# Kernel tuning notes

Hardware: AMD Instinct MI355X
Metric: run time of the kernel (lower is better)

Reference implementation:

```python
import jax, jax.numpy as jnp
import numpy as np

DIM = 512

def setup_inputs() -> dict:
    key = jax.random.key(0)
    ks = jax.random.split(key, 7)
    B, Nq, Nkv = 8, 1024, 4096
    prototype = jax.random.normal(ks[0], (B, Nq, DIM), dtype=jnp.float32)
    q_x = jax.random.normal(ks[1], (B, Nkv, DIM), dtype=jnp.float32)
    qry_attn_mask = jax.random.bernoulli(ks[2], 0.5, (B, Nkv))  # True = keep
    # Linear(dim, dim, bias=False) weights, torch convention y = x @ W.T
    s = 1.0 / np.sqrt(DIM)
    Wq = jax.random.uniform(ks[3], (DIM, DIM), jnp.float32, -s, s)
    Wk = jax.random.uniform(ks[4], (DIM, DIM), jnp.float32, -s, s)
    Wv = jax.random.uniform(ks[5], (DIM, DIM), jnp.float32, -s, s)
    Wproj = jax.random.uniform(ks[6], (DIM, DIM), jnp.float32, -s, s)
    return {"prototype": prototype, "q_x": q_x, "qry_attn_mask": qry_attn_mask,
            "Wq": Wq, "Wk": Wk, "Wv": Wv, "Wproj": Wproj}

def reference(prototype, q_x, qry_attn_mask, Wq, Wk, Wv, Wproj):
    scale = DIM ** (-0.5)
    q = jnp.einsum('bnd,ed->bne', prototype, Wq)          # [B,Nq,D]
    k = jnp.einsum('bmd,ed->bme', q_x, Wk)                # [B,Nkv,D]
    v = jnp.einsum('bmd,ed->bme', q_x, Wv)                # [B,Nkv,D]
    attn = jnp.einsum('bnd,bmd->bnm', q, k) * scale       # [B,Nq,Nkv]
    bias = (~qry_attn_mask).astype(attn.dtype)[:, None, :] * -10000.0
    attn = jax.nn.softmax(attn + bias, axis=-1)
    x = jnp.einsum('bnm,bmd->bnd', attn, v)
    x = jnp.einsum('bnd,ed->bne', x, Wproj)
    return x
```

## Files before the change

### kernel.cpp

```cpp
#include <hip/hip_runtime.h>
#include <hip/hip_bf16.h>
#include <stdint.h>


typedef __bf16 bf16;
typedef bf16 bf16x8 __attribute__((ext_vector_type(8)));
typedef bf16 bf16x4 __attribute__((ext_vector_type(4)));
typedef float f32x4 __attribute__((ext_vector_type(4)));

#define NB 8
#define NQ 1024
#define NKV 4096
#define DD 512
#define RT_LD 136

__device__ __forceinline__ void lds16(const bf16* g, bf16* l) {
  __builtin_amdgcn_global_load_lds(
      (const __attribute__((address_space(1))) unsigned int*)g,
      (__attribute__((address_space(3))) unsigned int*)l, 16, 0, 0);
}

__global__ void scan_mask(const void* __restrict__ mask,
                          int* __restrict__ idx, int* __restrict__ cnt,
                          int* __restrict__ kpad, float* __restrict__ denom) {
  const int b = blockIdx.x, tid = threadIdx.x;
  for (int i = tid; i < NQ; i += 256) denom[b * NQ + i] = 0.f;

  __shared__ int s0, s1;
  if (tid == 0) { s0 = 0; s1 = 0; }
  __syncthreads();
  {
    const unsigned* mw = (const unsigned*)mask;
    int b0 = 0, b1 = 0;
    for (int i = tid; i < 8192; i += 256) {
      unsigned v = mw[i];
      if (v > 1u) b0 = 1;
      if (v != 0u && v != 0x3F800000u) b1 = 1;
    }
    if (b0) atomicOr(&s0, 1);
    if (b1) atomicOr(&s1, 1);
  }
  __syncthreads();
  const int mode = (s0 == 0) ? 0 : ((s1 == 0) ? 1 : 2);

  __shared__ int ps[256];
  unsigned bits = 0;
  int c = 0;
  const int base = tid * 16;
  for (int i = 0; i < 16; ++i) {
    const int col = base + i;
    bool k;
    if (mode == 0)      k = ((const int*)mask)[b * NKV + col] != 0;
    else if (mode == 1) k = ((const float*)mask)[b * NKV + col] != 0.f;
    else                k = ((const unsigned char*)mask)[b * NKV + col] != 0;
    bits |= (unsigned)k << i;
    c += k;
  }
  ps[tid] = c;
  __syncthreads();
  for (int s = 1; s < 256; s <<= 1) {
    int v = (tid >= s) ? ps[tid - s] : 0;
    __syncthreads();
    ps[tid] += v;
    __syncthreads();
  }
  int off = ps[tid] - c;
  for (int i = 0; i < 16; ++i)
    if ((bits >> i) & 1) idx[b * NKV + off++] = base + i;
  if (tid == 255) {
    cnt[b] = ps[255];
    kpad[b] = (ps[255] + 127) & ~127;
  }
}

__global__ void prep(const float* __restrict__ qx, const int* __restrict__ idx,
                     const int* __restrict__ cnt, const int* __restrict__ kpad,
                     bf16* __restrict__ qc,
                     const float* __restrict__ proto, bf16* __restrict__ proto_b,
                     const float* __restrict__ Wq, const float* __restrict__ Wk,
                     const float* __restrict__ Wv, const float* __restrict__ Wp,
                     bf16* __restrict__ Wq_b, bf16* __restrict__ Wkv_b,
                     bf16* __restrict__ Wp_b) {
  const int blk = blockIdx.x, tid = threadIdx.x;
  if (blk < 2048) {
    const int b = blk >> 8, bx = blk & 255;
    const int wave = tid >> 6, lane = tid & 63;
    const int r0 = bx * 16 + wave * 4;
    const int n = cnt[b];
    const int kp = kpad[b];
#pragma unroll
    for (int j = 0; j < 4; ++j) {
      const int row = r0 + j;
      if (row >= kp) return;
      bf16x4* d = (bf16x4*)(qc + ((long)b * NKV + row) * DD) + lane;
      if (row < n) {
        const int src = idx[b * NKV + row];
        const float4* s = (const float4*)(qx + ((long)b * NKV + src) * DD) + lane;
        float4 v0 = s[0], v1 = s[64];
        bf16x4 o0, o1;
        o0.x = (bf16)v0.x; o0.y = (bf16)v0.y; o0.z = (bf16)v0.z; o0.w = (bf16)v0.w;
        o1.x = (bf16)v1.x; o1.y = (bf16)v1.y; o1.z = (bf16)v1.z; o1.w = (bf16)v1.w;
        d[0] = o0;
        d[64] = o1;
      } else {
        bf16x4 z;
        z.x = (bf16)0.f; z.y = (bf16)0.f; z.z = (bf16)0.f; z.w = (bf16)0.f;
        d[0] = z;
        d[64] = z;
      }
    }
  } else if (blk < 6144) {
    const int i = (blk - 2048) * 256 + tid;
    float4 v = ((const float4*)proto)[i];
    bf16x4 o;
    o.x = (bf16)v.x; o.y = (bf16)v.y; o.z = (bf16)v.z; o.w = (bf16)v.w;
    ((bf16x4*)proto_b)[i] = o;
  } else {
    const int j = (blk - 6144) * 256 + tid;
    const int w = j >> 16, r = j & 65535;
    const float* src = (w == 0) ? Wq : (w == 1) ? Wk : (w == 2) ? Wv : Wp;
    bf16x4* dst = (w == 0) ? (bf16x4*)Wq_b
                : (w == 3) ? (bf16x4*)Wp_b
                           : (bf16x4*)Wkv_b + (w == 2 ? 65536 : 0);
    float4 v = ((const float4*)src)[r];
    bf16x4 o;
    o.x = (bf16)v.x; o.y = (bf16)v.y; o.z = (bf16)v.z; o.w = (bf16)v.w;
    dst[r] = o;
  }
}

template <int EPI>
__global__ void __launch_bounds__(256, 2)
gemm_bt(const bf16* __restrict__ A, const bf16* __restrict__ Bw,
        void* __restrict__ Cp, void* __restrict__ Cp2,
        int N, int Klen, int Kstride,
        long sA, long sB, long sC,
        const int* __restrict__ cnt, const int* __restrict__ kpad,
        float* __restrict__ denom, float scale, int M) {
  __shared__ alignas(16) bf16 Smem[128 * RT_LD];
  bf16* As = Smem;
  bf16* Bs = Smem + 8192;
  bf16* Rt = Smem;
  const int tid = threadIdx.x;
  const int wave = tid >> 6, lane = tid & 63;
  const int l15 = lane & 15, l4 = lane >> 4;
  const int wm = (wave >> 1) * 64, wn = (wave & 1) * 64;
  const int bx = (EPI == 5) ? blockIdx.y : blockIdx.x;
  const int by = (EPI == 5) ? blockIdx.x : blockIdx.y;
  const int b = blockIdx.z;

  if constexpr (EPI == 2) {
    if (bx * 128 >= kpad[b]) return;
  } else if constexpr (EPI == 5) {
    const int bb = by >> 5, loc = (by & 31) * 128;
    if (loc >= kpad[bb]) return;
  }

  const bf16* Ab = A + (long)b * sA + (long)(by * 128) * Kstride;
  const bf16* Bb = Bw + (long)b * sB + (long)(bx * 128) * Kstride;

  const int srow = lane >> 2, scol = (lane & 3) * 8;
  const bf16* ag[4];
  const bf16* bg[4];
  bf16* al[4];
  bf16* bl[4];
#pragma unroll
  for (int i = 0; i < 4; ++i) {
    const int st = wave * 4 + i, rs = st >> 1, cs = st & 1;
    ag[i] = Ab + (long)(rs * 16 + srow) * Kstride + cs * 32 + scol;
    bg[i] = Bb + (long)(rs * 16 + srow) * Kstride + cs * 32 + scol;
    al[i] = As + st * 512;
    bl[i] = Bs + st * 512;
  }

  f32x4 acc[4][4] = {};

  for (int kt = 0; kt < Klen; kt += 64) {
    __syncthreads();
#pragma unroll
    for (int i = 0; i < 4; ++i) lds16(ag[i], al[i]);
#pragma unroll
    for (int i = 0; i < 4; ++i) lds16(bg[i], bl[i]);
#pragma unroll
    for (int i = 0; i < 4; ++i) { ag[i] += 64; bg[i] += 64; }
    __syncthreads();
    bf16x8 af0[4], af1[4], bf0[4], bf1[4];
    const int ra = (wave >> 1) * 4, rb = (wave & 1) * 4;
#pragma unroll
    for (int t = 0; t < 4; ++t) {
      af0[t] = *(const bf16x8*)(As + ((ra + t) * 2 + 0) * 512 + l15 * 32 + l4 * 8);
      af1[t] = *(const bf16x8*)(As + ((ra + t) * 2 + 1) * 512 + l15 * 32 + l4 * 8);
      bf0[t] = *(const bf16x8*)(Bs + ((rb + t) * 2 + 0) * 512 + l15 * 32 + l4 * 8);
      bf1[t] = *(const bf16x8*)(Bs + ((rb + t) * 2 + 1) * 512 + l15 * 32 + l4 * 8);
    }
#pragma unroll
    for (int mt = 0; mt < 4; ++mt)
#pragma unroll
      for (int nt = 0; nt < 4; ++nt) {
        acc[mt][nt] = __builtin_amdgcn_mfma_f32_16x16x32_bf16(af0[mt], bf0[nt],
                                                              acc[mt][nt], 0, 0, 0);
        acc[mt][nt] = __builtin_amdgcn_mfma_f32_16x16x32_bf16(af1[mt], bf1[nt],
                                                              acc[mt][nt], 0, 0, 0);
      }
  }

  const int rowBase = by * 128 + wm;
  const int colBase = bx * 128 + wn;
  const int tR = by * 128;
  const int tC = bx * 128;

  __syncthreads();

  if constexpr (EPI == 2) {
    bf16* C = (bf16*)Cp + (long)b * sC;
    const int nkeep = cnt[b];
    float rs[4][4];
#pragma unroll
    for (int mt = 0; mt < 4; ++mt)
#pragma unroll
      for (int r = 0; r < 4; ++r) rs[mt][r] = 0.f;
#pragma unroll
    for (int nt = 0; nt < 4; ++nt) {
      const bool keep = (colBase + nt * 16 + l15) < nkeep;
#pragma unroll
      for (int mt = 0; mt < 4; ++mt)
#pragma unroll
        for (int r = 0; r < 4; ++r) {
          float p = keep ? __expf(acc[mt][nt][r] * scale) : 0.f;
          rs[mt][r] += p;
          Rt[(wm + mt * 16 + l4 * 4 + r) * RT_LD + wn + nt * 16 + l15] = (bf16)p;
        }
    }
#pragma unroll
    for (int mt = 0; mt < 4; ++mt)
#pragma unroll
      for (int r = 0; r < 4; ++r) {
        float v = rs[mt][r];
        v += __shfl_xor(v, 1, 64);
        v += __shfl_xor(v, 2, 64);
        v += __shfl_xor(v, 4, 64);
        v += __shfl_xor(v, 8, 64);
        if (l15 == 0)
          atomicAdd(&denom[b * M + rowBase + mt * 16 + l4 * 4 + r], v);
      }
    __syncthreads();
    const int r0 = tid >> 2, cq = (tid & 3) * 32;
#pragma unroll
    for (int h = 0; h < 128; h += 64)
#pragma unroll
      for (int j = 0; j < 4; ++j) {
        bf16x8 v = *(const bf16x8*)(Rt + (r0 + h) * RT_LD + cq + j * 8);
        *(bf16x8*)(C + (long)(tR + r0 + h) * N + tC + cq + j * 8) = v;
      }
  } else if constexpr (EPI == 0) {
    bf16* C = (bf16*)Cp;
#pragma unroll
    for (int mt = 0; mt < 4; ++mt)
#pragma unroll
      for (int nt = 0; nt < 4; ++nt)
#pragma unroll
        for (int r = 0; r < 4; ++r)
          Rt[(wm + mt * 16 + l4 * 4 + r) * RT_LD + wn + nt * 16 + l15] =
              (bf16)acc[mt][nt][r];
    __syncthreads();
    const int r0 = tid >> 2, cq = (tid & 3) * 32;
#pragma unroll
    for (int h = 0; h < 128; h += 64)
#pragma unroll
      for (int j = 0; j < 4; ++j) {
        bf16x8 v = *(const bf16x8*)(Rt + (r0 + h) * RT_LD + cq + j * 8);
        *(bf16x8*)(C + (long)(tR + r0 + h) * N + tC + cq + j * 8) = v;
      }
  } else if constexpr (EPI == 4) {
    float* C = (float*)Cp;
#pragma unroll
    for (int mt = 0; mt < 4; ++mt)
#pragma unroll
      for (int nt = 0; nt < 4; ++nt)
#pragma unroll
        for (int r = 0; r < 4; ++r)
          C[(long)(tR + wm + mt * 16 + l4 * 4 + r) * N + tC + wn + nt * 16 + l15] =
              acc[mt][nt][r];
  } else {
    if (tC < 512) {
      bf16* C = (bf16*)Cp;
#pragma unroll
      for (int mt = 0; mt < 4; ++mt)
#pragma unroll
        for (int nt = 0; nt < 4; ++nt)
#pragma unroll
          for (int r = 0; r < 4; ++r)
            Rt[(wm + mt * 16 + l4 * 4 + r) * RT_LD + wn + nt * 16 + l15] =
                (bf16)acc[mt][nt][r];
      __syncthreads();
      const int r0 = tid >> 2, cq = (tid & 3) * 32;
#pragma unroll
      for (int h = 0; h < 128; h += 64)
#pragma unroll
        for (int j = 0; j < 4; ++j) {
          bf16x8 v = *(const bf16x8*)(Rt + (r0 + h) * RT_LD + cq + j * 8);
          *(bf16x8*)(C + (long)(tR + r0 + h) * 512 + tC + cq + j * 8) = v;
        }
    } else {
      bf16* C = (bf16*)Cp2;
#pragma unroll
      for (int mt = 0; mt < 4; ++mt) {
        const int r0 = wm + mt * 16 + l4 * 4;
#pragma unroll
        for (int nt = 0; nt < 4; ++nt) {
          const int cloc = wn + nt * 16 + l15;
          bf16x4 o;
          o.x = (bf16)acc[mt][nt][0]; o.y = (bf16)acc[mt][nt][1];
          o.z = (bf16)acc[mt][nt][2]; o.w = (bf16)acc[mt][nt][3];
          *(bf16x4*)(Rt + cloc * RT_LD + r0) = o;
        }
      }
      __syncthreads();
      const int bb = tR >> 12, kvloc = tR & 4095;
      const int d0 = tid >> 2, kvq = (tid & 3) * 32;
#pragma unroll
      for (int h = 0; h < 128; h += 64)
#pragma unroll
        for (int j = 0; j < 4; ++j) {
          bf16x8 v = *(const bf16x8*)(Rt + (d0 + h) * RT_LD + kvq + j * 8);
          *(bf16x8*)(C + (long)bb * DD * NKV + (long)(tC - 512 + d0 + h) * NKV +
                     kvloc + kvq + j * 8) = v;
        }
    }
  }
}

__global__ void __launch_bounds__(256, 4)
pv_direct(const bf16* __restrict__ P, const bf16* __restrict__ vT,
          const float* __restrict__ denom, const int* __restrict__ kpad,
          bf16* __restrict__ x) {
  __shared__ alignas(16) bf16 Smem[12288];
  bf16* As = Smem;
  bf16* Bs = Smem + 4096;
  bf16* Rt = Smem;
  const int tid = threadIdx.x;
  const int wave = tid >> 6, lane = tid & 63;
  const int l15 = lane & 15, l4 = lane >> 4;
  const int wm = (wave >> 1) * 32, wn = (wave & 1) * 64;
  const int qB = blockIdx.x * 64;
  const int dB = blockIdx.y * 128;
  const int b = blockIdx.z;
  const int Kb = kpad[b];

  const bf16* Ab = P + (long)b * NQ * NKV + (long)qB * NKV;
  const bf16* Bb = vT + (long)b * DD * NKV + (long)dB * NKV;

  const int srow = lane >> 2, scol = (lane & 3) * 8;
  const bf16* ag[2];
  const bf16* bg[4];
  bf16* al[2];
  bf16* bl[4];
#pragma unroll
  for (int i = 0; i < 2; ++i) {
    const int st = wave * 2 + i, rs = st >> 1, cs = st & 1;
    ag[i] = Ab + (long)(rs * 16 + srow) * NKV + cs * 32 + scol;
    al[i] = As + st * 512;
  }
#pragma unroll
  for (int i = 0; i < 4; ++i) {
    const int st = wave * 4 + i, rs = st >> 1, cs = st & 1;
    bg[i] = Bb + (long)(rs * 16 + srow) * NKV + cs * 32 + scol;
    bl[i] = Bs + st * 512;
  }

  f32x4 acc[2][4] = {};

  for (int kt = 0; kt < Kb; kt += 64) {
    __syncthreads();
#pragma unroll
    for (int i = 0; i < 2; ++i) lds16(ag[i], al[i]);
#pragma unroll
    for (int i = 0; i < 4; ++i) lds16(bg[i], bl[i]);
#pragma unroll
    for (int i = 0; i < 2; ++i) ag[i] += 64;
#pragma unroll
    for (int i = 0; i < 4; ++i) bg[i] += 64;
    __syncthreads();
    bf16x8 af0[2], af1[2], bf0[4], bf1[4];
    const int ra = (wave >> 1) * 2, rb = (wave & 1) * 4;
#pragma unroll
    for (int t = 0; t < 2; ++t) {
      af0[t] = *(const bf16x8*)(As + ((ra + t) * 2 + 0) * 512 + l15 * 32 + l4 * 8);
      af1[t] = *(const bf16x8*)(As + ((ra + t) * 2 + 1) * 512 + l15 * 32 + l4 * 8);
    }
#pragma unroll
    for (int t = 0; t < 4; ++t) {
      bf0[t] = *(const bf16x8*)(Bs + ((rb + t) * 2 + 0) * 512 + l15 * 32 + l4 * 8);
      bf1[t] = *(const bf16x8*)(Bs + ((rb + t) * 2 + 1) * 512 + l15 * 32 + l4 * 8);
    }
#pragma unroll
    for (int mt = 0; mt < 2; ++mt)
#pragma unroll
      for (int nt = 0; nt < 4; ++nt) {
        acc[mt][nt] = __builtin_amdgcn_mfma_f32_16x16x32_bf16(af0[mt], bf0[nt],
                                                              acc[mt][nt], 0, 0, 0);
        acc[mt][nt] = __builtin_amdgcn_mfma_f32_16x16x32_bf16(af1[mt], bf1[nt],
                                                              acc[mt][nt], 0, 0, 0);
      }
  }

  __syncthreads();
#pragma unroll
  for (int mt = 0; mt < 2; ++mt)
#pragma unroll
    for (int r = 0; r < 4; ++r) {
      const int row = wm + mt * 16 + l4 * 4 + r;
      const float inv = 1.0f / denom[b * NQ + qB + row];
#pragma unroll
      for (int nt = 0; nt < 4; ++nt)
        Rt[row * RT_LD + wn + nt * 16 + l15] = (bf16)(acc[mt][nt][r] * inv);
    }
  __syncthreads();
  const int r0 = tid >> 2, cq = (tid & 3) * 32;
#pragma unroll
  for (int j = 0; j < 4; ++j) {
    bf16x8 v = *(const bf16x8*)(Rt + r0 * RT_LD + cq + j * 8);
    *(bf16x8*)(x + (long)(b * NQ + qB + r0) * DD + dB + cq + j * 8) = v;
  }
}

extern "C" void kernel_launch(void* const* d_in, const int* in_sizes, int n_in,
                              void* d_out, int out_size, void* d_ws, size_t ws_size,
                              hipStream_t stream) {
  const float* proto = (const float*)d_in[0];
  const float* qx    = (const float*)d_in[1];
  const void*  mask  = d_in[2];
  const float* Wq    = (const float*)d_in[3];
  const float* Wk    = (const float*)d_in[4];
  const float* Wv    = (const float*)d_in[5];
  const float* Wproj = (const float*)d_in[6];
  float* out = (float*)d_out;

  char* w = (char*)d_ws;
  int*   cnt   = (int*)(w + 64);
  int*   kpadA = (int*)(w + 128);
  float* denom = (float*)(w + 4096);
  size_t off = 65536;
  bf16* Wq_b  = (bf16*)(w + off); off += (size_t)DD * DD * 2;
  bf16* Wkv_b = (bf16*)(w + off); off += (size_t)DD * DD * 4;
  bf16* Wp_b  = (bf16*)(w + off); off += (size_t)DD * DD * 2;
  int*  idx   = (int*)(w + off);  off += (size_t)NB * NKV * 4;
  bf16* q_b   = (bf16*)(w + off); off += (size_t)NB * NQ * DD * 2;
  bf16* k_b   = (bf16*)(w + off); off += (size_t)NB * NKV * DD * 2;
  bf16* vT_b  = (bf16*)(w + off); off += (size_t)NB * NKV * DD * 2;
  bf16* x_b   = (bf16*)(w + off); off += (size_t)NB * NQ * DD * 2;
  size_t off_pp = off;
  bf16* proto_b = (bf16*)(w + off); off += (size_t)NB * NQ * DD * 2;
  bf16* qc_b    = (bf16*)(w + off);
  bf16* P       = (bf16*)(w + off_pp);

  scan_mask<<<8, 256, 0, stream>>>(mask, idx, cnt, kpadA, denom);
  prep<<<7168, 256, 0, stream>>>(qx, idx, cnt, kpadA, qc_b,
                                 proto, proto_b, Wq, Wk, Wv, Wproj,
                                 Wq_b, Wkv_b, Wp_b);

  const float scale = 0.04419417382415922f;

  gemm_bt<0><<<dim3(4, 64, 1), 256, 0, stream>>>(
      proto_b, Wq_b, q_b, nullptr, DD, DD, DD, 0L, 0L, 0L,
      cnt, kpadA, nullptr, 0.f, 0);
  gemm_bt<5><<<dim3(256, 8, 1), 256, 0, stream>>>(
      qc_b, Wkv_b, k_b, vT_b, 1024, DD, DD, 0L, 0L, 0L,
      cnt, kpadA, nullptr, 0.f, 0);
  gemm_bt<2><<<dim3(NKV / 128, NQ / 128, NB), 256, 0, stream>>>(
      q_b, k_b, P, nullptr, NKV, DD, DD,
      (long)NQ * DD, (long)NKV * DD, (long)NQ * NKV,
      cnt, kpadA, denom, scale, NQ);
  pv_direct<<<dim3(16, 4, 8), 256, 0, stream>>>(P, vT_b, denom, kpadA, x_b);
  gemm_bt<4><<<dim3(4, 64, 1), 256, 0, stream>>>(
      x_b, Wp_b, out, nullptr, DD, DD, DD, 0L, 0L, 0L,
      cnt, kpadA, nullptr, 0.f, 0);
}
```

Baseline: 313.8 us.

## Double-buffer LDS tiles in gemm_bt and pv_direct to overlap loads with MFMA

Both GEMM kernels now prefetch the next K tile into a second LDS buffer while the current tile is being consumed by MFMAs. This uses one barrier per iteration instead of two. The aim is to hide global-to-LDS load latency behind compute. In exchange, shared memory per block doubles and pv_direct's launch-bounds occupancy hint drops from 4 to 3, which may reduce how many blocks are resident.

```diff
diff --git a/kernel.cpp b/kernel.cpp
--- a/kernel.cpp
+++ b/kernel.cpp
@@ -129,6 +129,7 @@
   }
 }
 
+#define GB_DBUF 16384
 template <int EPI>
 __global__ void __launch_bounds__(256, 2)
 gemm_bt(const bf16* __restrict__ A, const bf16* __restrict__ Bw,
@@ -137,7 +138,7 @@
         long sA, long sB, long sC,
         const int* __restrict__ cnt, const int* __restrict__ kpad,
         float* __restrict__ denom, float scale, int M) {
-  __shared__ alignas(16) bf16 Smem[128 * RT_LD];
+  __shared__ alignas(16) bf16 Smem[32768];
   bf16* As = Smem;
   bf16* Bs = Smem + 8192;
   bf16* Rt = Smem;
@@ -175,23 +176,35 @@
 
   f32x4 acc[4][4] = {};
 
+#pragma unroll
+  for (int i = 0; i < 4; ++i) lds16(ag[i], al[i]);
+#pragma unroll
+  for (int i = 0; i < 4; ++i) lds16(bg[i], bl[i]);
+#pragma unroll
+  for (int i = 0; i < 4; ++i) { ag[i] += 64; bg[i] += 64; }
+  __syncthreads();
+
+  int cur = 0;
   for (int kt = 0; kt < Klen; kt += 64) {
-    __syncthreads();
-#pragma unroll
-    for (int i = 0; i < 4; ++i) lds16(ag[i], al[i]);
-#pragma unroll
-    for (int i = 0; i < 4; ++i) lds16(bg[i], bl[i]);
-#pragma unroll
-    for (int i = 0; i < 4; ++i) { ag[i] += 64; bg[i] += 64; }
-    __syncthreads();
+    const bf16* Ac = As + cur * GB_DBUF;
+    const bf16* Bc = Bs + cur * GB_DBUF;
     bf16x8 af0[4], af1[4], bf0[4], bf1[4];
     const int ra = (wave >> 1) * 4, rb = (wave & 1) * 4;
 #pragma unroll
     for (int t = 0; t < 4; ++t) {
-      af0[t] = *(const bf16x8*)(As + ((ra + t) * 2 + 0) * 512 + l15 * 32 + l4 * 8);
-      af1[t] = *(const bf16x8*)(As + ((ra + t) * 2 + 1) * 512 + l15 * 32 + l4 * 8);
-      bf0[t] = *(const bf16x8*)(Bs + ((rb + t) * 2 + 0) * 512 + l15 * 32 + l4 * 8);
-      bf1[t] = *(const bf16x8*)(Bs + ((rb + t) * 2 + 1) * 512 + l15 * 32 + l4 * 8);
+      af0[t] = *(const bf16x8*)(Ac + ((ra + t) * 2 + 0) * 512 + l15 * 32 + l4 * 8);
+      af1[t] = *(const bf16x8*)(Ac + ((ra + t) * 2 + 1) * 512 + l15 * 32 + l4 * 8);
+      bf0[t] = *(const bf16x8*)(Bc + ((rb + t) * 2 + 0) * 512 + l15 * 32 + l4 * 8);
+      bf1[t] = *(const bf16x8*)(Bc + ((rb + t) * 2 + 1) * 512 + l15 * 32 + l4 * 8);
+    }
+    if (kt + 64 < Klen) {
+      const int nb = (cur ^ 1) * GB_DBUF;
+#pragma unroll
+      for (int i = 0; i < 4; ++i) lds16(ag[i], al[i] + nb);
+#pragma unroll
+      for (int i = 0; i < 4; ++i) lds16(bg[i], bl[i] + nb);
+#pragma unroll
+      for (int i = 0; i < 4; ++i) { ag[i] += 64; bg[i] += 64; }
     }
 #pragma unroll
     for (int mt = 0; mt < 4; ++mt)
@@ -202,14 +215,14 @@
         acc[mt][nt] = __builtin_amdgcn_mfma_f32_16x16x32_bf16(af1[mt], bf1[nt],
                                                               acc[mt][nt], 0, 0, 0);
       }
+    __syncthreads();
+    cur ^= 1;
   }
 
   const int rowBase = by * 128 + wm;
   const int colBase = bx * 128 + wn;
   const int tR = by * 128;
   const int tC = bx * 128;
-
-  __syncthreads();
 
   if constexpr (EPI == 2) {
     bf16* C = (bf16*)Cp + (long)b * sC;
@@ -330,11 +343,12 @@
   }
 }
 
-__global__ void __launch_bounds__(256, 4)
+#define PV_DBUF 12288
+__global__ void __launch_bounds__(256, 3)
 pv_direct(const bf16* __restrict__ P, const bf16* __restrict__ vT,
           const float* __restrict__ denom, const int* __restrict__ kpad,
           bf16* __restrict__ x) {
-  __shared__ alignas(16) bf16 Smem[12288];
+  __shared__ alignas(16) bf16 Smem[24576];
   bf16* As = Smem;
   bf16* Bs = Smem + 4096;
   bf16* Rt = Smem;
@@ -370,28 +384,42 @@
 
   f32x4 acc[2][4] = {};
 
+#pragma unroll
+  for (int i = 0; i < 2; ++i) lds16(ag[i], al[i]);
+#pragma unroll
+  for (int i = 0; i < 4; ++i) lds16(bg[i], bl[i]);
+#pragma unroll
+  for (int i = 0; i < 2; ++i) ag[i] += 64;
+#pragma unroll
+  for (int i = 0; i < 4; ++i) bg[i] += 64;
+  __syncthreads();
+
+  int cur = 0;
   for (int kt = 0; kt < Kb; kt += 64) {
-    __syncthreads();
-#pragma unroll
-    for (int i = 0; i < 2; ++i) lds16(ag[i], al[i]);
-#pragma unroll
-    for (int i = 0; i < 4; ++i) lds16(bg[i], bl[i]);
-#pragma unroll
-    for (int i = 0; i < 2; ++i) ag[i] += 64;
-#pragma unroll
-    for (int i = 0; i < 4; ++i) bg[i] += 64;
-    __syncthreads();
+    const bf16* Ac = As + cur * PV_DBUF;
+    const bf16* Bc = Bs + cur * PV_DBUF;
     bf16x8 af0[2], af1[2], bf0[4], bf1[4];
     const int ra = (wave >> 1) * 2, rb = (wave & 1) * 4;
 #pragma unroll
     for (int t = 0; t < 2; ++t) {
-      af0[t] = *(const bf16x8*)(As + ((ra + t) * 2 + 0) * 512 + l15 * 32 + l4 * 8);
-      af1[t] = *(const bf16x8*)(As + ((ra + t) * 2 + 1) * 512 + l15 * 32 + l4 * 8);
+      af0[t] = *(const bf16x8*)(Ac + ((ra + t) * 2 + 0) * 512 + l15 * 32 + l4 * 8);
+      af1[t] = *(const bf16x8*)(Ac + ((ra + t) * 2 + 1) * 512 + l15 * 32 + l4 * 8);
     }
 #pragma unroll
     for (int t = 0; t < 4; ++t) {
-      bf0[t] = *(const bf16x8*)(Bs + ((rb + t) * 2 + 0) * 512 + l15 * 32 + l4 * 8);
-      bf1[t] = *(const bf16x8*)(Bs + ((rb + t) * 2 + 1) * 512 + l15 * 32 + l4 * 8);
+      bf0[t] = *(const bf16x8*)(Bc + ((rb + t) * 2 + 0) * 512 + l15 * 32 + l4 * 8);
+      bf1[t] = *(const bf16x8*)(Bc + ((rb + t) * 2 + 1) * 512 + l15 * 32 + l4 * 8);
+    }
+    if (kt + 64 < Kb) {
+      const int nb = (cur ^ 1) * PV_DBUF;
+#pragma unroll
+      for (int i = 0; i < 2; ++i) lds16(ag[i], al[i] + nb);
+#pragma unroll
+      for (int i = 0; i < 4; ++i) lds16(bg[i], bl[i] + nb);
+#pragma unroll
+      for (int i = 0; i < 2; ++i) ag[i] += 64;
+#pragma unroll
+      for (int i = 0; i < 4; ++i) bg[i] += 64;
     }
 #pragma unroll
     for (int mt = 0; mt < 2; ++mt)
@@ -402,9 +430,10 @@
         acc[mt][nt] = __builtin_amdgcn_mfma_f32_16x16x32_bf16(af1[mt], bf1[nt],
                                                               acc[mt][nt], 0, 0, 0);
       }
-  }
-
-  __syncthreads();
+    __syncthreads();
+    cur ^= 1;
+  }
+
 #pragma unroll
   for (int mt = 0; mt < 2; ++mt)
 #pragma unroll
```

Result: slower. 327.8 us (+4.5%).

## Triple-buffer K=32 stages in GEMM and PV kernels with async LDS loads

Applied to the files above, without the earlier changes.

Replaces the single-buffered K=64 load/compute loop in gemm_bt and pv_direct with a three-stage ring of K=32 tiles. Direct-to-LDS loads are issued two stages ahead, with explicit vmcnt waits and a single barrier per step. This is meant to overlap global-memory latency with MFMA work instead of serialising them behind two barriers per iteration. It also raises the gemm launch bound to 3 blocks per CU. The cost is more shared memory per block, and only one barrier per step guards against overwriting a buffer that a slower wave may still be reading.

```diff
diff --git a/kernel.cpp b/kernel.cpp
--- a/kernel.cpp
+++ b/kernel.cpp
@@ -130,16 +130,14 @@
 }
 
 template <int EPI>
-__global__ void __launch_bounds__(256, 2)
+__global__ void __launch_bounds__(256, 3)
 gemm_bt(const bf16* __restrict__ A, const bf16* __restrict__ Bw,
         void* __restrict__ Cp, void* __restrict__ Cp2,
         int N, int Klen, int Kstride,
         long sA, long sB, long sC,
         const int* __restrict__ cnt, const int* __restrict__ kpad,
         float* __restrict__ denom, float scale, int M) {
-  __shared__ alignas(16) bf16 Smem[128 * RT_LD];
-  bf16* As = Smem;
-  bf16* Bs = Smem + 8192;
+  __shared__ alignas(16) bf16 Smem[24576];
   bf16* Rt = Smem;
   const int tid = threadIdx.x;
   const int wave = tid >> 6, lane = tid & 63;
@@ -160,57 +158,64 @@
   const bf16* Bb = Bw + (long)b * sB + (long)(bx * 128) * Kstride;
 
   const int srow = lane >> 2, scol = (lane & 3) * 8;
-  const bf16* ag[4];
-  const bf16* bg[4];
-  bf16* al[4];
-  bf16* bl[4];
-#pragma unroll
-  for (int i = 0; i < 4; ++i) {
-    const int st = wave * 4 + i, rs = st >> 1, cs = st & 1;
-    ag[i] = Ab + (long)(rs * 16 + srow) * Kstride + cs * 32 + scol;
-    bg[i] = Bb + (long)(rs * 16 + srow) * Kstride + cs * 32 + scol;
-    al[i] = As + st * 512;
-    bl[i] = Bs + st * 512;
-  }
+  const int c0 = wave * 2, c1 = wave * 2 + 1;
+  const bf16* g0 = Ab + (long)(c0 * 16 + srow) * Kstride + scol;
+  const bf16* g1 = Ab + (long)(c1 * 16 + srow) * Kstride + scol;
+  const bf16* g2 = Bb + (long)(c0 * 16 + srow) * Kstride + scol;
+  const bf16* g3 = Bb + (long)(c1 * 16 + srow) * Kstride + scol;
+  bf16* l0 = Smem + c0 * 512;
+  bf16* l1 = Smem + c1 * 512;
+  bf16* l2 = Smem + 4096 + c0 * 512;
+  bf16* l3 = Smem + 4096 + c1 * 512;
 
   f32x4 acc[4][4] = {};
-
-  for (int kt = 0; kt < Klen; kt += 64) {
-    __syncthreads();
-#pragma unroll
-    for (int i = 0; i < 4; ++i) lds16(ag[i], al[i]);
-#pragma unroll
-    for (int i = 0; i < 4; ++i) lds16(bg[i], bl[i]);
-#pragma unroll
-    for (int i = 0; i < 4; ++i) { ag[i] += 64; bg[i] += 64; }
-    __syncthreads();
-    bf16x8 af0[4], af1[4], bf0[4], bf1[4];
-    const int ra = (wave >> 1) * 4, rb = (wave & 1) * 4;
-#pragma unroll
-    for (int t = 0; t < 4; ++t) {
-      af0[t] = *(const bf16x8*)(As + ((ra + t) * 2 + 0) * 512 + l15 * 32 + l4 * 8);
-      af1[t] = *(const bf16x8*)(As + ((ra + t) * 2 + 1) * 512 + l15 * 32 + l4 * 8);
-      bf0[t] = *(const bf16x8*)(Bs + ((rb + t) * 2 + 0) * 512 + l15 * 32 + l4 * 8);
-      bf1[t] = *(const bf16x8*)(Bs + ((rb + t) * 2 + 1) * 512 + l15 * 32 + l4 * 8);
+  const int nt = Klen >> 5;
+
+#define GSTAGE(bb)                                            \
+  do {                                                        \
+    const int o_ = (bb) * 8192;                               \
+    lds16(g0, l0 + o_); lds16(g1, l1 + o_);                   \
+    lds16(g2, l2 + o_); lds16(g3, l3 + o_);                   \
+    g0 += 32; g1 += 32; g2 += 32; g3 += 32;                   \
+  } while (0)
+
+  GSTAGE(0);
+  GSTAGE(1);
+  int rd = 0, wr = 2;
+  for (int t = 0; t < nt; ++t) {
+    if (t + 1 < nt) {
+      asm volatile("s_waitcnt vmcnt(4)" ::: "memory");
+    } else {
+      asm volatile("s_waitcnt vmcnt(0)" ::: "memory");
+    }
+    __builtin_amdgcn_s_barrier();
+    __builtin_amdgcn_sched_barrier(0);
+    if (t + 2 < nt) GSTAGE(wr);
+    wr = (wr == 2) ? 0 : wr + 1;
+    const bf16* Ac = Smem + rd * 8192;
+    const bf16* Bc = Ac + 4096;
+    rd = (rd == 2) ? 0 : rd + 1;
+    bf16x8 af[4], bfr[4];
+#pragma unroll
+    for (int t2 = 0; t2 < 4; ++t2) {
+      af[t2]  = *(const bf16x8*)(Ac + (wm + t2 * 16 + l15) * 32 + l4 * 8);
+      bfr[t2] = *(const bf16x8*)(Bc + (wn + t2 * 16 + l15) * 32 + l4 * 8);
     }
 #pragma unroll
     for (int mt = 0; mt < 4; ++mt)
 #pragma unroll
-      for (int nt = 0; nt < 4; ++nt) {
-        acc[mt][nt] = __builtin_amdgcn_mfma_f32_16x16x32_bf16(af0[mt], bf0[nt],
-                                                              acc[mt][nt], 0, 0, 0);
-        acc[mt][nt] = __builtin_amdgcn_mfma_f32_16x16x32_bf16(af1[mt], bf1[nt],
-                                                              acc[mt][nt], 0, 0, 0);
-      }
-  }
+      for (int nt2 = 0; nt2 < 4; ++nt2)
+        acc[mt][nt2] = __builtin_amdgcn_mfma_f32_16x16x32_bf16(af[mt], bfr[nt2],
+                                                               acc[mt][nt2], 0, 0, 0);
+  }
+#undef GSTAGE
+  __syncthreads();
 
   const int rowBase = by * 128 + wm;
   const int colBase = bx * 128 + wn;
   const int tR = by * 128;
   const int tC = bx * 128;
 
-  __syncthreads();
-
   if constexpr (EPI == 2) {
     bf16* C = (bf16*)Cp + (long)b * sC;
     const int nkeep = cnt[b];
@@ -220,15 +225,15 @@
 #pragma unroll
       for (int r = 0; r < 4; ++r) rs[mt][r] = 0.f;
 #pragma unroll
-    for (int nt = 0; nt < 4; ++nt) {
-      const bool keep = (colBase + nt * 16 + l15) < nkeep;
+    for (int nt2 = 0; nt2 < 4; ++nt2) {
+      const bool keep = (colBase + nt2 * 16 + l15) < nkeep;
 #pragma unroll
       for (int mt = 0; mt < 4; ++mt)
 #pragma unroll
         for (int r = 0; r < 4; ++r) {
-          float p = keep ? __expf(acc[mt][nt][r] * scale) : 0.f;
+          float p = keep ? __expf(acc[mt][nt2][r] * scale) : 0.f;
           rs[mt][r] += p;
-          Rt[(wm + mt * 16 + l4 * 4 + r) * RT_LD + wn + nt * 16 + l15] = (bf16)p;
+          Rt[(wm + mt * 16 + l4 * 4 + r) * RT_LD + wn + nt2 * 16 + l15] = (bf16)p;
         }
     }
 #pragma unroll
@@ -257,11 +262,11 @@
 #pragma unroll
     for (int mt = 0; mt < 4; ++mt)
 #pragma unroll
-      for (int nt = 0; nt < 4; ++nt)
+      for (int nt2 = 0; nt2 < 4; ++nt2)
 #pragma unroll
         for (int r = 0; r < 4; ++r)
-          Rt[(wm + mt * 16 + l4 * 4 + r) * RT_LD + wn + nt * 16 + l15] =
-              (bf16)acc[mt][nt][r];
+          Rt[(wm + mt * 16 + l4 * 4 + r) * RT_LD + wn + nt2 * 16 + l15] =
+              (bf16)acc[mt][nt2][r];
     __syncthreads();
     const int r0 = tid >> 2, cq = (tid & 3) * 32;
 #pragma unroll
@@ -276,22 +281,22 @@
 #pragma unroll
     for (int mt = 0; mt < 4; ++mt)
 #pragma unroll
-      for (int nt = 0; nt < 4; ++nt)
+      for (int nt2 = 0; nt2 < 4; ++nt2)
 #pragma unroll
         for (int r = 0; r < 4; ++r)
-          C[(long)(tR + wm + mt * 16 + l4 * 4 + r) * N + tC + wn + nt * 16 + l15] =
-              acc[mt][nt][r];
+          C[(long)(tR + wm + mt * 16 + l4 * 4 + r) * N + tC + wn + nt2 * 16 + l15] =
+              acc[mt][nt2][r];
   } else {
     if (tC < 512) {
       bf16* C = (bf16*)Cp;
 #pragma unroll
       for (int mt = 0; mt < 4; ++mt)
 #pragma unroll
-        for (int nt = 0; nt < 4; ++nt)
+        for (int nt2 = 0; nt2 < 4; ++nt2)
 #pragma unroll
           for (int r = 0; r < 4; ++r)
-            Rt[(wm + mt * 16 + l4 * 4 + r) * RT_LD + wn + nt * 16 + l15] =
-                (bf16)acc[mt][nt][r];
+            Rt[(wm + mt * 16 + l4 * 4 + r) * RT_LD + wn + nt2 * 16 + l15] =
+                (bf16)acc[mt][nt2][r];
       __syncthreads();
       const int r0 = tid >> 2, cq = (tid & 3) * 32;
 #pragma unroll
@@ -307,11 +312,11 @@
       for (int mt = 0; mt < 4; ++mt) {
         const int r0 = wm + mt * 16 + l4 * 4;
 #pragma unroll
-        for (int nt = 0; nt < 4; ++nt) {
-          const int cloc = wn + nt * 16 + l15;
+        for (int nt2 = 0; nt2 < 4; ++nt2) {
+          const int cloc = wn + nt2 * 16 + l15;
           bf16x4 o;
-          o.x = (bf16)acc[mt][nt][0]; o.y = (bf16)acc[mt][nt][1];
-          o.z = (bf16)acc[mt][nt][2]; o.w = (bf16)acc[mt][nt][3];
+          o.x = (bf16)acc[mt][nt2][0]; o.y = (bf16)acc[mt][nt2][1];
+          o.z = (bf16)acc[mt][nt2][2]; o.w = (bf16)acc[mt][nt2][3];
           *(bf16x4*)(Rt + cloc * RT_LD + r0) = o;
         }
       }
@@ -334,9 +339,7 @@
 pv_direct(const bf16* __restrict__ P, const bf16* __restrict__ vT,
           const float* __restrict__ denom, const int* __restrict__ kpad,
           bf16* __restrict__ x) {
-  __shared__ alignas(16) bf16 Smem[12288];
-  bf16* As = Smem;
-  bf16* Bs = Smem + 4096;
+  __shared__ alignas(16) bf16 Smem[18432];
   bf16* Rt = Smem;
   const int tid = threadIdx.x;
   const int wave = tid >> 6, lane = tid & 63;
@@ -351,60 +354,58 @@
   const bf16* Bb = vT + (long)b * DD * NKV + (long)dB * NKV;
 
   const int srow = lane >> 2, scol = (lane & 3) * 8;
-  const bf16* ag[2];
-  const bf16* bg[4];
-  bf16* al[2];
-  bf16* bl[4];
-#pragma unroll
-  for (int i = 0; i < 2; ++i) {
-    const int st = wave * 2 + i, rs = st >> 1, cs = st & 1;
-    ag[i] = Ab + (long)(rs * 16 + srow) * NKV + cs * 32 + scol;
-    al[i] = As + st * 512;
-  }
-#pragma unroll
-  for (int i = 0; i < 4; ++i) {
-    const int st = wave * 4 + i, rs = st >> 1, cs = st & 1;
-    bg[i] = Bb + (long)(rs * 16 + srow) * NKV + cs * 32 + scol;
-    bl[i] = Bs + st * 512;
-  }
+  const int c0 = wave * 2, c1 = wave * 2 + 1;
+  const bf16* ga  = Ab + (long)(wave * 16 + srow) * NKV + scol;
+  const bf16* gb0 = Bb + (long)(c0 * 16 + srow) * NKV + scol;
+  const bf16* gb1 = Bb + (long)(c1 * 16 + srow) * NKV + scol;
+  bf16* la  = Smem + wave * 512;
+  bf16* lb0 = Smem + 2048 + c0 * 512;
+  bf16* lb1 = Smem + 2048 + c1 * 512;
 
   f32x4 acc[2][4] = {};
-
-  for (int kt = 0; kt < Kb; kt += 64) {
-    __syncthreads();
-#pragma unroll
-    for (int i = 0; i < 2; ++i) lds16(ag[i], al[i]);
-#pragma unroll
-    for (int i = 0; i < 4; ++i) lds16(bg[i], bl[i]);
-#pragma unroll
-    for (int i = 0; i < 2; ++i) ag[i] += 64;
-#pragma unroll
-    for (int i = 0; i < 4; ++i) bg[i] += 64;
-    __syncthreads();
-    bf16x8 af0[2], af1[2], bf0[4], bf1[4];
-    const int ra = (wave >> 1) * 2, rb = (wave & 1) * 4;
-#pragma unroll
-    for (int t = 0; t < 2; ++t) {
-      af0[t] = *(const bf16x8*)(As + ((ra + t) * 2 + 0) * 512 + l15 * 32 + l4 * 8);
-      af1[t] = *(const bf16x8*)(As + ((ra + t) * 2 + 1) * 512 + l15 * 32 + l4 * 8);
-    }
-#pragma unroll
-    for (int t = 0; t < 4; ++t) {
-      bf0[t] = *(const bf16x8*)(Bs + ((rb + t) * 2 + 0) * 512 + l15 * 32 + l4 * 8);
-      bf1[t] = *(const bf16x8*)(Bs + ((rb + t) * 2 + 1) * 512 + l15 * 32 + l4 * 8);
-    }
+  const int nt = Kb >> 5;
+
+#define PSTAGE(bb)                                           \
+  do {                                                       \
+    const int o_ = (bb) * 6144;                              \
+    lds16(ga, la + o_); lds16(gb0, lb0 + o_);                \
+    lds16(gb1, lb1 + o_);                                    \
+    ga += 32; gb0 += 32; gb1 += 32;                          \
+  } while (0)
+
+  PSTAGE(0);
+  PSTAGE(1);
+  int rd = 0, wr = 2;
+  for (int t = 0; t < nt; ++t) {
+    if (t + 1 < nt) {
+      asm volatile("s_waitcnt vmcnt(3)" ::: "memory");
+    } else {
+      asm volatile("s_waitcnt vmcnt(0)" ::: "memory");
+    }
+    __builtin_amdgcn_s_barrier();
+    __builtin_amdgcn_sched_barrier(0);
+    if (t + 2 < nt) PSTAGE(wr);
+    wr = (wr == 2) ? 0 : wr + 1;
+    const bf16* Ac = Smem + rd * 6144;
+    const bf16* Bc = Ac + 2048;
+    rd = (rd == 2) ? 0 : rd + 1;
+    bf16x8 af[2], bfr[4];
+#pragma unroll
+    for (int t2 = 0; t2 < 2; ++t2)
+      af[t2] = *(const bf16x8*)(Ac + (wm + t2 * 16 + l15) * 32 + l4 * 8);
+#pragma unroll
+    for (int t2 = 0; t2 < 4; ++t2)
+      bfr[t2] = *(const bf16x8*)(Bc + (wn + t2 * 16 + l15) * 32 + l4 * 8);
 #pragma unroll
     for (int mt = 0; mt < 2; ++mt)
 #pragma unroll
-      for (int nt = 0; nt < 4; ++nt) {
-        acc[mt][nt] = __builtin_amdgcn_mfma_f32_16x16x32_bf16(af0[mt], bf0[nt],
-                                                              acc[mt][nt], 0, 0, 0);
-        acc[mt][nt] = __builtin_amdgcn_mfma_f32_16x16x32_bf16(af1[mt], bf1[nt],
-                                                              acc[mt][nt], 0, 0, 0);
-      }
-  }
-
-  __syncthreads();
+      for (int nt2 = 0; nt2 < 4; ++nt2)
+        acc[mt][nt2] = __builtin_amdgcn_mfma_f32_16x16x32_bf16(af[mt], bfr[nt2],
+                                                               acc[mt][nt2], 0, 0, 0);
+  }
+#undef PSTAGE
+  __syncthreads();
+
 #pragma unroll
   for (int mt = 0; mt < 2; ++mt)
 #pragma unroll
@@ -412,8 +413,8 @@
       const int row = wm + mt * 16 + l4 * 4 + r;
       const float inv = 1.0f / denom[b * NQ + qB + row];
 #pragma unroll
-      for (int nt = 0; nt < 4; ++nt)
-        Rt[row * RT_LD + wn + nt * 16 + l15] = (bf16)(acc[mt][nt][r] * inv);
+      for (int nt2 = 0; nt2 < 4; ++nt2)
+        Rt[row * RT_LD + wn + nt2 * 16 + l15] = (bf16)(acc[mt][nt2][r] * inv);
     }
   __syncthreads();
   const int r0 = tid >> 2, cq = (tid & 3) * 32;
```

After: 308.3 us. No clear change (-1.7%).

## Halve K-tile to 32 and split epilogue staging to cut LDS for occupancy

Applied to the files above, without the earlier changes.

Both GEMM kernels now stage a K-depth of 32 instead of 64 per iteration, shrinking the A/B LDS buffers. The epilogues write the 128x128 result tile through LDS in two 64-row (or 64-column) halves so the staging buffer fits in the smaller allocation. Launch bounds are raised to 6 blocks per CU to use the freed LDS for more resident waves. The cost is twice as many barrier-separated loop iterations with less MFMA work per barrier, extra barriers in the epilogue, and tighter per-thread register budgets that may cause spills.

```diff
diff --git a/kernel.cpp b/kernel.cpp
--- a/kernel.cpp
+++ b/kernel.cpp
@@ -130,16 +130,16 @@
 }
 
 template <int EPI>
-__global__ void __launch_bounds__(256, 2)
+__global__ void __launch_bounds__(256, 6)
 gemm_bt(const bf16* __restrict__ A, const bf16* __restrict__ Bw,
         void* __restrict__ Cp, void* __restrict__ Cp2,
         int N, int Klen, int Kstride,
         long sA, long sB, long sC,
         const int* __restrict__ cnt, const int* __restrict__ kpad,
         float* __restrict__ denom, float scale, int M) {
-  __shared__ alignas(16) bf16 Smem[128 * RT_LD];
+  __shared__ alignas(16) bf16 Smem[8704];
   bf16* As = Smem;
-  bf16* Bs = Smem + 8192;
+  bf16* Bs = Smem + 4096;
   bf16* Rt = Smem;
   const int tid = threadIdx.x;
   const int wave = tid >> 6, lane = tid & 63;
@@ -159,55 +159,48 @@
   const bf16* Ab = A + (long)b * sA + (long)(by * 128) * Kstride;
   const bf16* Bb = Bw + (long)b * sB + (long)(bx * 128) * Kstride;
 
-  const int srow = lane >> 2, scol = (lane & 3) * 8;
-  const bf16* ag[4];
-  const bf16* bg[4];
-  bf16* al[4];
-  bf16* bl[4];
-#pragma unroll
-  for (int i = 0; i < 4; ++i) {
-    const int st = wave * 4 + i, rs = st >> 1, cs = st & 1;
-    ag[i] = Ab + (long)(rs * 16 + srow) * Kstride + cs * 32 + scol;
-    bg[i] = Bb + (long)(rs * 16 + srow) * Kstride + cs * 32 + scol;
-    al[i] = As + st * 512;
-    bl[i] = Bs + st * 512;
-  }
+  const int c0 = wave * 2, c1 = wave * 2 + 1;
+  const int srow = lane >> 2;
+  const int scol = (lane & 3) * 8;
+  const bf16* ag0 = Ab + (long)(c0 * 16 + srow) * Kstride + scol;
+  const bf16* ag1 = Ab + (long)(c1 * 16 + srow) * Kstride + scol;
+  const bf16* bg0 = Bb + (long)(c0 * 16 + srow) * Kstride + scol;
+  const bf16* bg1 = Bb + (long)(c1 * 16 + srow) * Kstride + scol;
+  bf16* al0 = As + c0 * 512;
+  bf16* al1 = As + c1 * 512;
+  bf16* bl0 = Bs + c0 * 512;
+  bf16* bl1 = Bs + c1 * 512;
 
   f32x4 acc[4][4] = {};
 
-  for (int kt = 0; kt < Klen; kt += 64) {
-    __syncthreads();
-#pragma unroll
-    for (int i = 0; i < 4; ++i) lds16(ag[i], al[i]);
-#pragma unroll
-    for (int i = 0; i < 4; ++i) lds16(bg[i], bl[i]);
-#pragma unroll
-    for (int i = 0; i < 4; ++i) { ag[i] += 64; bg[i] += 64; }
-    __syncthreads();
-    bf16x8 af0[4], af1[4], bf0[4], bf1[4];
-    const int ra = (wave >> 1) * 4, rb = (wave & 1) * 4;
-#pragma unroll
-    for (int t = 0; t < 4; ++t) {
-      af0[t] = *(const bf16x8*)(As + ((ra + t) * 2 + 0) * 512 + l15 * 32 + l4 * 8);
-      af1[t] = *(const bf16x8*)(As + ((ra + t) * 2 + 1) * 512 + l15 * 32 + l4 * 8);
-      bf0[t] = *(const bf16x8*)(Bs + ((rb + t) * 2 + 0) * 512 + l15 * 32 + l4 * 8);
-      bf1[t] = *(const bf16x8*)(Bs + ((rb + t) * 2 + 1) * 512 + l15 * 32 + l4 * 8);
-    }
+  for (int kt = 0; kt < Klen; kt += 32) {
+    __syncthreads();
+    lds16(ag0, al0);
+    lds16(ag1, al1);
+    lds16(bg0, bl0);
+    lds16(bg1, bl1);
+    ag0 += 32; ag1 += 32; bg0 += 32; bg1 += 32;
+    __syncthreads();
+    bf16x8 af[4], bfr[4];
+#pragma unroll
+    for (int t = 0; t < 4; ++t)
+      af[t] = *(const bf16x8*)(As + (wm + t * 16 + l15) * 32 + l4 * 8);
+#pragma unroll
+    for (int t = 0; t < 4; ++t)
+      bfr[t] = *(const bf16x8*)(Bs + (wn + t * 16 + l15) * 32 + l4 * 8);
 #pragma unroll
     for (int mt = 0; mt < 4; ++mt)
 #pragma unroll
-      for (int nt = 0; nt < 4; ++nt) {
-        acc[mt][nt] = __builtin_amdgcn_mfma_f32_16x16x32_bf16(af0[mt], bf0[nt],
+      for (int nt = 0; nt < 4; ++nt)
+        acc[mt][nt] = __builtin_amdgcn_mfma_f32_16x16x32_bf16(af[mt], bfr[nt],
                                                               acc[mt][nt], 0, 0, 0);
-        acc[mt][nt] = __builtin_amdgcn_mfma_f32_16x16x32_bf16(af1[mt], bf1[nt],
-                                                              acc[mt][nt], 0, 0, 0);
-      }
   }
 
   const int rowBase = by * 128 + wm;
   const int colBase = bx * 128 + wn;
   const int tR = by * 128;
   const int tC = bx * 128;
+  const int r0 = tid >> 2, cq = (tid & 3) * 32;
 
   __syncthreads();
 
@@ -225,11 +218,8 @@
 #pragma unroll
       for (int mt = 0; mt < 4; ++mt)
 #pragma unroll
-        for (int r = 0; r < 4; ++r) {
-          float p = keep ? __expf(acc[mt][nt][r] * scale) : 0.f;
-          rs[mt][r] += p;
-          Rt[(wm + mt * 16 + l4 * 4 + r) * RT_LD + wn + nt * 16 + l15] = (bf16)p;
-        }
+        for (int r = 0; r < 4; ++r)
+          rs[mt][r] += keep ? __expf(acc[mt][nt][r] * scale) : 0.f;
     }
 #pragma unroll
     for (int mt = 0; mt < 4; ++mt)
@@ -243,34 +233,51 @@
         if (l15 == 0)
           atomicAdd(&denom[b * M + rowBase + mt * 16 + l4 * 4 + r], v);
       }
-    __syncthreads();
-    const int r0 = tid >> 2, cq = (tid & 3) * 32;
-#pragma unroll
-    for (int h = 0; h < 128; h += 64)
+#pragma unroll
+    for (int ph = 0; ph < 2; ++ph) {
+      if (wm == ph * 64) {
+#pragma unroll
+        for (int nt = 0; nt < 4; ++nt) {
+          const bool keep = (colBase + nt * 16 + l15) < nkeep;
+#pragma unroll
+          for (int mt = 0; mt < 4; ++mt)
+#pragma unroll
+            for (int r = 0; r < 4; ++r) {
+              float p = keep ? __expf(acc[mt][nt][r] * scale) : 0.f;
+              Rt[(mt * 16 + l4 * 4 + r) * RT_LD + wn + nt * 16 + l15] = (bf16)p;
+            }
+        }
+      }
+      __syncthreads();
 #pragma unroll
       for (int j = 0; j < 4; ++j) {
-        bf16x8 v = *(const bf16x8*)(Rt + (r0 + h) * RT_LD + cq + j * 8);
-        *(bf16x8*)(C + (long)(tR + r0 + h) * N + tC + cq + j * 8) = v;
-      }
+        bf16x8 v = *(const bf16x8*)(Rt + r0 * RT_LD + cq + j * 8);
+        *(bf16x8*)(C + (long)(tR + ph * 64 + r0) * N + tC + cq + j * 8) = v;
+      }
+      __syncthreads();
+    }
   } else if constexpr (EPI == 0) {
     bf16* C = (bf16*)Cp;
 #pragma unroll
-    for (int mt = 0; mt < 4; ++mt)
-#pragma unroll
-      for (int nt = 0; nt < 4; ++nt)
-#pragma unroll
-        for (int r = 0; r < 4; ++r)
-          Rt[(wm + mt * 16 + l4 * 4 + r) * RT_LD + wn + nt * 16 + l15] =
-              (bf16)acc[mt][nt][r];
-    __syncthreads();
-    const int r0 = tid >> 2, cq = (tid & 3) * 32;
-#pragma unroll
-    for (int h = 0; h < 128; h += 64)
+    for (int ph = 0; ph < 2; ++ph) {
+      if (wm == ph * 64) {
+#pragma unroll
+        for (int mt = 0; mt < 4; ++mt)
+#pragma unroll
+          for (int nt = 0; nt < 4; ++nt)
+#pragma unroll
+            for (int r = 0; r < 4; ++r)
+              Rt[(mt * 16 + l4 * 4 + r) * RT_LD + wn + nt * 16 + l15] =
+                  (bf16)acc[mt][nt][r];
+      }
+      __syncthreads();
 #pragma unroll
       for (int j = 0; j < 4; ++j) {
-        bf16x8 v = *(const bf16x8*)(Rt + (r0 + h) * RT_LD + cq + j * 8);
-        *(bf16x8*)(C + (long)(tR + r0 + h) * N + tC + cq + j * 8) = v;
-      }
+        bf16x8 v = *(const bf16x8*)(Rt + r0 * RT_LD + cq + j * 8);
+        *(bf16x8*)(C + (long)(tR + ph * 64 + r0) * N + tC + cq + j * 8) = v;
+      }
+      __syncthreads();
+    }
   } else if constexpr (EPI == 4) {
     float* C = (float*)Cp;
 #pragma unroll
@@ -285,58 +292,64 @@
     if (tC < 512) {
       bf16* C = (bf16*)Cp;
 #pragma unroll
-      for (int mt = 0; mt < 4; ++mt)
-#pragma unroll
-        for (int nt = 0; nt < 4; ++nt)
-#pragma unroll
-          for (int r = 0; r < 4; ++r)
-            Rt[(wm + mt * 16 + l4 * 4 + r) * RT_LD + wn + nt * 16 + l15] =
-                (bf16)acc[mt][nt][r];
-      __syncthreads();
-      const int r0 = tid >> 2, cq = (tid & 3) * 32;
-#pragma unroll
-      for (int h = 0; h < 128; h += 64)
+      for (int ph = 0; ph < 2; ++ph) {
+        if (wm == ph * 64) {
+#pragma unroll
+          for (int mt = 0; mt < 4; ++mt)
+#pragma unroll
+            for (int nt = 0; nt < 4; ++nt)
+#pragma unroll
+              for (int r = 0; r < 4; ++r)
+                Rt[(mt * 16 + l4 * 4 + r) * RT_LD + wn + nt * 16 + l15] =
+                    (bf16)acc[mt][nt][r];
+        }
+        __syncthreads();
 #pragma unroll
         for (int j = 0; j < 4; ++j) {
-          bf16x8 v = *(const bf16x8*)(Rt + (r0 + h) * RT_LD + cq + j * 8);
-          *(bf16x8*)(C + (long)(tR + r0 + h) * 512 + tC + cq + j * 8) = v;
+          bf16x8 v = *(const bf16x8*)(Rt + r0 * RT_LD + cq + j * 8);
+          *(bf16x8*)(C + (long)(tR + ph * 64 + r0) * 512 + tC + cq + j * 8) = v;
         }
+        __syncthreads();
+      }
     } else {
       bf16* C = (bf16*)Cp2;
-#pragma unroll
-      for (int mt = 0; mt < 4; ++mt) {
-        const int r0 = wm + mt * 16 + l4 * 4;
-#pragma unroll
-        for (int nt = 0; nt < 4; ++nt) {
-          const int cloc = wn + nt * 16 + l15;
-          bf16x4 o;
-          o.x = (bf16)acc[mt][nt][0]; o.y = (bf16)acc[mt][nt][1];
-          o.z = (bf16)acc[mt][nt][2]; o.w = (bf16)acc[mt][nt][3];
-          *(bf16x4*)(Rt + cloc * RT_LD + r0) = o;
+      const int bb = tR >> 12, kvloc = tR & 4095;
+#pragma unroll
+      for (int ph = 0; ph < 2; ++ph) {
+        if (wn == ph * 64) {
+#pragma unroll
+          for (int mt = 0; mt < 4; ++mt) {
+            const int rr = wm + mt * 16 + l4 * 4;
+#pragma unroll
+            for (int nt = 0; nt < 4; ++nt) {
+              const int cloc = nt * 16 + l15;
+              bf16x4 o;
+              o.x = (bf16)acc[mt][nt][0]; o.y = (bf16)acc[mt][nt][1];
+              o.z = (bf16)acc[mt][nt][2]; o.w = (bf16)acc[mt][nt][3];
+              *(bf16x4*)(Rt + cloc * RT_LD + rr) = o;
+            }
+          }
         }
-      }
-      __syncthreads();
-      const int bb = tR >> 12, kvloc = tR & 4095;
-      const int d0 = tid >> 2, kvq = (tid & 3) * 32;
-#pragma unroll
-      for (int h = 0; h < 128; h += 64)
+        __syncthreads();
 #pragma unroll
         for (int j = 0; j < 4; ++j) {
-          bf16x8 v = *(const bf16x8*)(Rt + (d0 + h) * RT_LD + kvq + j * 8);
-          *(bf16x8*)(C + (long)bb * DD * NKV + (long)(tC - 512 + d0 + h) * NKV +
-                     kvloc + kvq + j * 8) = v;
+          bf16x8 v = *(const bf16x8*)(Rt + r0 * RT_LD + cq + j * 8);
+          *(bf16x8*)(C + (long)bb * DD * NKV +
+                     (long)(tC - 512 + ph * 64 + r0) * NKV + kvloc + cq + j * 8) = v;
         }
-    }
-  }
-}
-
-__global__ void __launch_bounds__(256, 4)
+        __syncthreads();
+      }
+    }
+  }
+}
+
+__global__ void __launch_bounds__(256, 6)
 pv_direct(const bf16* __restrict__ P, const bf16* __restrict__ vT,
           const float* __restrict__ denom, const int* __restrict__ kpad,
           bf16* __restrict__ x) {
-  __shared__ alignas(16) bf16 Smem[12288];
+  __shared__ alignas(16) bf16 Smem[8704];
   bf16* As = Smem;
-  bf16* Bs = Smem + 4096;
+  bf16* Bs = Smem + 2048;
   bf16* Rt = Smem;
   const int tid = threadIdx.x;
   const int wave = tid >> 6, lane = tid & 63;
@@ -351,57 +364,36 @@
   const bf16* Bb = vT + (long)b * DD * NKV + (long)dB * NKV;
 
   const int srow = lane >> 2, scol = (lane & 3) * 8;
-  const bf16* ag[2];
-  const bf16* bg[4];
-  bf16* al[2];
-  bf16* bl[4];
-#pragma unroll
-  for (int i = 0; i < 2; ++i) {
-    const int st = wave * 2 + i, rs = st >> 1, cs = st & 1;
-    ag[i] = Ab + (long)(rs * 16 + srow) * NKV + cs * 32 + scol;
-    al[i] = As + st * 512;
-  }
-#pragma unroll
-  for (int i = 0; i < 4; ++i) {
-    const int st = wave * 4 + i, rs = st >> 1, cs = st & 1;
-    bg[i] = Bb + (long)(rs * 16 + srow) * NKV + cs * 32 + scol;
-    bl[i] = Bs + st * 512;
-  }
+  const int c0 = wave * 2, c1 = wave * 2 + 1;
+  const bf16* ag  = Ab + (long)(wave * 16 + srow) * NKV + scol;
+  const bf16* bg0 = Bb + (long)(c0 * 16 + srow) * NKV + scol;
+  const bf16* bg1 = Bb + (long)(c1 * 16 + srow) * NKV + scol;
+  bf16* la  = As + wave * 512;
+  bf16* lb0 = Bs + c0 * 512;
+  bf16* lb1 = Bs + c1 * 512;
 
   f32x4 acc[2][4] = {};
 
-  for (int kt = 0; kt < Kb; kt += 64) {
-    __syncthreads();
-#pragma unroll
-    for (int i = 0; i < 2; ++i) lds16(ag[i], al[i]);
-#pragma unroll
-    for (int i = 0; i < 4; ++i) lds16(bg[i], bl[i]);
-#pragma unroll
-    for (int i = 0; i < 2; ++i) ag[i] += 64;
-#pragma unroll
-    for (int i = 0; i < 4; ++i) bg[i] += 64;
-    __syncthreads();
-    bf16x8 af0[2], af1[2], bf0[4], bf1[4];
-    const int ra = (wave >> 1) * 2, rb = (wave & 1) * 4;
-#pragma unroll
-    for (int t = 0; t < 2; ++t) {
-      af0[t] = *(const bf16x8*)(As + ((ra + t) * 2 + 0) * 512 + l15 * 32 + l4 * 8);
-      af1[t] = *(const bf16x8*)(As + ((ra + t) * 2 + 1) * 512 + l15 * 32 + l4 * 8);
-    }
-#pragma unroll
-    for (int t = 0; t < 4; ++t) {
-      bf0[t] = *(const bf16x8*)(Bs + ((rb + t) * 2 + 0) * 512 + l15 * 32 + l4 * 8);
-      bf1[t] = *(const bf16x8*)(Bs + ((rb + t) * 2 + 1) * 512 + l15 * 32 + l4 * 8);
-    }
+  for (int kt = 0; kt < Kb; kt += 32) {
+    __syncthreads();
+    lds16(ag, la);
+    lds16(bg0, lb0);
+    lds16(bg1, lb1);
+    ag += 32; bg0 += 32; bg1 += 32;
+    __syncthreads();
+    bf16x8 af[2], bfr[4];
+#pragma unroll
+    for (int t = 0; t < 2; ++t)
+      af[t] = *(const bf16x8*)(As + (wm + t * 16 + l15) * 32 + l4 * 8);
+#pragma unroll
+    for (int t = 0; t < 4; ++t)
+      bfr[t] = *(const bf16x8*)(Bs + (wn + t * 16 + l15) * 32 + l4 * 8);
 #pragma unroll
     for (int mt = 0; mt < 2; ++mt)
 #pragma unroll
-      for (int nt = 0; nt < 4; ++nt) {
-        acc[mt][nt] = __builtin_amdgcn_mfma_f32_16x16x32_bf16(af0[mt], bf0[nt],
+      for (int nt = 0; nt < 4; ++nt)
+        acc[mt][nt] = __builtin_amdgcn_mfma_f32_16x16x32_bf16(af[mt], bfr[nt],
                                                               acc[mt][nt], 0, 0, 0);
-        acc[mt][nt] = __builtin_amdgcn_mfma_f32_16x16x32_bf16(af1[mt], bf1[nt],
-                                                              acc[mt][nt], 0, 0, 0);
-      }
   }
 
   __syncthreads();
```

New measurement: 679.9 us. 2.17x slower.
